# Kernel optimization log

Hardware: AMD Instinct MI355X
Metric: run time of the kernel (lower is better)

Reference implementation:

```python
import jax, jax.numpy as jnp
import numpy as np

N_NODES = 50000
N_EDGES = 800000
IN_FEATS = 128
OUT_FEATS = 16
NUM_HEADS = 8
NEG_SLOPE = 0.2


def setup_inputs() -> dict:
    key = jax.random.key(0)
    k1, k2, k3, k4, k5 = jax.random.split(key, 5)
    feat = jax.random.normal(k1, (N_NODES, IN_FEATS), dtype=jnp.float32)
    src = jax.random.randint(k2, (N_EDGES,), 0, N_NODES, dtype=jnp.int32)
    dst = jax.random.randint(k3, (N_EDGES,), 0, N_NODES, dtype=jnp.int32)
    # fc weight stored as [in, H*Dout] so y = x @ W (equivalent to torch Linear)
    W = jax.random.normal(k4, (IN_FEATS, NUM_HEADS * OUT_FEATS), dtype=jnp.float32) * 0.05
    attn_weights = jax.random.normal(k5, (2 * NUM_HEADS * OUT_FEATS,), dtype=jnp.float32) * 0.1
    bias = jnp.zeros((NUM_HEADS * OUT_FEATS,), dtype=jnp.float32)
    return {"feat": feat, "W": W, "attn_weights": attn_weights, "bias": bias,
            "src": src, "dst": dst}


def reference(feat, W, attn_weights, bias, src, dst):
    H, D = NUM_HEADS, OUT_FEATS
    N = feat.shape[0]
    # Linear projection: [N, H, D]
    h = (feat @ W).reshape(N, H, D)
    a = attn_weights.reshape(2, H, D)
    # per-node attention logits per head
    e_src = jnp.einsum("nhd,hd->nh", h, a[0])  # source side
    e_dst = jnp.einsum("nhd,hd->nh", h, a[1])  # destination side
    # per-edge scores: [E, H]
    e = e_src[src] + e_dst[dst]
    e = jnp.where(e > 0, e, NEG_SLOPE * e)  # LeakyReLU
    # segment softmax over incoming edges of each dst node
    m = jax.ops.segment_max(e, dst, num_segments=N)          # [N, H]
    m = jnp.where(jnp.isfinite(m), m, 0.0)
    ex = jnp.exp(e - m[dst])                                  # [E, H]
    denom = jax.ops.segment_sum(ex, dst, num_segments=N)     # [N, H]
    alpha = ex / jnp.where(denom[dst] > 0, denom[dst], 1.0)  # [E, H]
    # weighted aggregation of source features: [N, H, D]
    out = jax.ops.segment_sum(alpha[:, :, None] * h[src], dst, num_segments=N)
    out = out + bias.reshape(1, H, D)
    return out
```

## Files before the change

### kernel.cpp

```cpp
#include <hip/hip_runtime.h>
#include <hip/hip_bf16.h>

#define H_HEADS 8
#define D_OUT 16
#define C_FEATS 128
#define NEG_SLOPE 0.2f

typedef __attribute__((ext_vector_type(8))) short short8;
typedef __attribute__((ext_vector_type(4))) float f32x4;

__device__ inline unsigned short f2bf(float f) {
    __hip_bfloat16 b = __float2bfloat16(f);
    return *reinterpret_cast<unsigned short*>(&b);
}
__device__ inline float bf2f(unsigned short u) {
    return __uint_as_float((unsigned)u << 16);
}
__device__ inline float bf_lo(unsigned u) { return __uint_as_float(u << 16); }
__device__ inline float bf_hi(unsigned u) { return __uint_as_float(u & 0xffff0000u); }

__global__ __launch_bounds__(256) void k_prep(const float* __restrict__ W,
                                              unsigned short* __restrict__ Wfh,
                                              unsigned short* __restrict__ Wfl,
                                              int* __restrict__ deg, int N) {
    const int b = blockIdx.x, t = threadIdx.x;
    if (b < 8) {
        const int idx = b * 256 + t;
        const int frag = idx >> 6, lane = idx & 63;
        const int kc = frag >> 3, nt = frag & 7;
        const int kb = kc * 32 + ((lane >> 4) << 3);
        const int col = nt * 16 + (lane & 15);
        unsigned short hs[8], ls[8];
#pragma unroll
        for (int i = 0; i < 8; ++i) {
            const float x = W[(size_t)(kb + i) * C_FEATS + col];
            const unsigned short hh = f2bf(x);
            hs[i] = hh;
            ls[i] = f2bf(x - bf2f(hh));
        }
        uint4 uh, ul;
        uh.x = hs[0] | ((unsigned)hs[1] << 16);
        uh.y = hs[2] | ((unsigned)hs[3] << 16);
        uh.z = hs[4] | ((unsigned)hs[5] << 16);
        uh.w = hs[6] | ((unsigned)hs[7] << 16);
        ul.x = ls[0] | ((unsigned)ls[1] << 16);
        ul.y = ls[2] | ((unsigned)ls[3] << 16);
        ul.z = ls[4] | ((unsigned)ls[5] << 16);
        ul.w = ls[6] | ((unsigned)ls[7] << 16);
        *reinterpret_cast<uint4*>(&Wfh[(size_t)idx * 8]) = uh;
        *reinterpret_cast<uint4*>(&Wfl[(size_t)idx * 8]) = ul;
    } else {
        const int i = (b - 8) * 256 + t;
        if (i < N) deg[i] = 0;
    }
}

__global__ __launch_bounds__(256) void k_deg_rank(const int* __restrict__ dst,
                                                  int* __restrict__ deg,
                                                  int* __restrict__ rank, int E) {
    const int e = blockIdx.x * 256 + threadIdx.x;
    if (e < E)
        rank[e] = atomicAdd(&deg[dst[e]], 1);
}

__global__ __launch_bounds__(512) void k_gemm(
    const float* __restrict__ feat, const unsigned short* __restrict__ Wfh,
    const unsigned short* __restrict__ Wfl, const float* __restrict__ aw,
    unsigned short* __restrict__ h16, float* __restrict__ es,
    float* __restrict__ ed, int N) {
    const int t = threadIdx.x;
    __shared__ uint4 sW[4096];
    {
        const uint4* gh = reinterpret_cast<const uint4*>(Wfh);
        const uint4* gl = reinterpret_cast<const uint4*>(Wfl);
#pragma unroll
        for (int i = 0; i < 4; ++i) {
            const int j = t + i * 512;
            sW[j] = gh[j];
            sW[j + 2048] = gl[j];
        }
    }
    __syncthreads();

    const int bid = blockIdx.x;
    const int w = t >> 6, lane = t & 63;
    const int rbase = bid * 128 + w * 16;
    const int rowA = rbase + (lane & 15);
    const int ko = (lane >> 4) << 3;
    const bool rv = rowA < N;
    const float* fr = feat + (size_t)rowA * C_FEATS;

    f32x4 acc[8];
#pragma unroll
    for (int nt = 0; nt < 8; ++nt)
#pragma unroll
        for (int j = 0; j < 4; ++j) acc[nt][j] = 0.f;

#pragma unroll
    for (int kc = 0; kc < 4; ++kc) {
        float4 x0 = make_float4(0.f, 0.f, 0.f, 0.f), x1 = x0;
        if (rv) {
            x0 = *reinterpret_cast<const float4*>(fr + kc * 32 + ko);
            x1 = *reinterpret_cast<const float4*>(fr + kc * 32 + ko + 4);
        }
        const float xs[8] = {x0.x, x0.y, x0.z, x0.w, x1.x, x1.y, x1.z, x1.w};
        short8 ah, al;
#pragma unroll
        for (int i = 0; i < 8; ++i) {
            const unsigned short hh = f2bf(xs[i]);
            ah[i] = (short)hh;
            al[i] = (short)f2bf(xs[i] - bf2f(hh));
        }
#pragma unroll
        for (int nt = 0; nt < 8; ++nt) {
            const int fi = (kc * 8 + nt) * 64 + lane;
            const short8 bh = *reinterpret_cast<const short8*>(&sW[fi]);
            const short8 bl = *reinterpret_cast<const short8*>(&sW[fi + 2048]);
            acc[nt] = __builtin_amdgcn_mfma_f32_16x16x32_bf16(ah, bh, acc[nt], 0, 0, 0);
            acc[nt] = __builtin_amdgcn_mfma_f32_16x16x32_bf16(al, bh, acc[nt], 0, 0, 0);
            acc[nt] = __builtin_amdgcn_mfma_f32_16x16x32_bf16(ah, bl, acc[nt], 0, 0, 0);
        }
    }
    const int r0 = rbase + ((lane >> 4) << 2);
    const int colc = lane & 15;
#pragma unroll
    for (int nt = 0; nt < 8; ++nt) {
#pragma unroll
        for (int r = 0; r < 4; ++r) {
            const int row = r0 + r;
            if (row < N)
                h16[(size_t)row * C_FEATS + nt * 16 + colc] = f2bf(acc[nt][r]);
        }
    }
#pragma unroll
    for (int nt = 0; nt < 8; ++nt) {
        const float wa = aw[nt * 16 + colc];
        const float wb = aw[C_FEATS + nt * 16 + colc];
#pragma unroll
        for (int r = 0; r < 4; ++r) {
            float pe = acc[nt][r] * wa;
            float pd = acc[nt][r] * wb;
#pragma unroll
            for (int msk = 1; msk <= 8; msk <<= 1) {
                pe += __shfl_xor(pe, msk, 64);
                pd += __shfl_xor(pd, msk, 64);
            }
            const int row = r0 + r;
            if (colc == 0 && row < N) {
                es[(size_t)row * H_HEADS + nt] = pe;
                ed[(size_t)row * H_HEADS + nt] = pd;
            }
        }
    }
}

__global__ void k_bsum(const int* __restrict__ deg, int* __restrict__ bsum, int N) {
    int i = blockIdx.x * 256 + threadIdx.x;
    int v = (i < N) ? deg[i] : 0;
#pragma unroll
    for (int m = 1; m < 64; m <<= 1) v += __shfl_xor(v, m, 64);
    __shared__ int ws[4];
    if ((threadIdx.x & 63) == 0) ws[threadIdx.x >> 6] = v;
    __syncthreads();
    if (threadIdx.x == 0) bsum[blockIdx.x] = ws[0] + ws[1] + ws[2] + ws[3];
}

__device__ inline int block_scan_incl(int v) {
    int lane = threadIdx.x & 63, w = threadIdx.x >> 6;
    int x = v;
#pragma unroll
    for (int d = 1; d < 64; d <<= 1) {
        int u = __shfl_up(x, d, 64);
        if (lane >= d) x += u;
    }
    __shared__ int wsum[4];
    if (lane == 63) wsum[w] = x;
    __syncthreads();
    int add = 0;
    for (int k = 0; k < w; ++k) add += wsum[k];
    return x + add;
}

__global__ void k_scanb(const int* __restrict__ bsum, int* __restrict__ bpre,
                        int NB, int* __restrict__ offs, int N) {
    int t = threadIdx.x;
    int v = (t < NB) ? bsum[t] : 0;
    int incl = block_scan_incl(v);
    if (t < NB) bpre[t] = incl - v;
    if (t == NB - 1) offs[N] = incl;
}

__global__ void k_scanc(const int* __restrict__ deg, const int* __restrict__ bpre,
                        int* __restrict__ offs, int N) {
    int i = blockIdx.x * 256 + threadIdx.x;
    int v = (i < N) ? deg[i] : 0;
    int incl = block_scan_incl(v);
    int excl = incl - v + bpre[blockIdx.x];
    if (i < N) offs[i] = excl;
}

__global__ void k_scatter(const int* __restrict__ src, const int* __restrict__ dst,
                          const int* __restrict__ rank, const int* __restrict__ offs,
                          int* __restrict__ ssorted, int E) {
    int e = blockIdx.x * 256 + threadIdx.x;
    if (e < E)
        ssorted[offs[dst[e]] + rank[e]] = src[e];
}

__global__ __launch_bounds__(256) void k_agg(const unsigned short* __restrict__ h16,
                                             const float* __restrict__ es,
                                             const float* __restrict__ ed,
                                             const int* __restrict__ offs,
                                             const int* __restrict__ ssorted,
                                             const float* __restrict__ bias,
                                             float* __restrict__ out, int N) {
    const int wid = threadIdx.x >> 6, lane = threadIdx.x & 63;
    const int n = blockIdx.x * 4 + wid;
    if (n >= N) return;
    const int beg = offs[n];
    const int deg = offs[n + 1] - beg;

    const int hh = lane >> 3, j0 = lane & 7;
    const float edv = ed[(size_t)n * H_HEADS + hh];

    const int cl = lane & 15, q = lane >> 4;
    const int ah = cl >> 1;
    const int ab = ah << 3;
    float acc[8];
#pragma unroll
    for (int k = 0; k < 8; ++k) acc[k] = 0.f;

    float m = -1e30f, s = 0.f;

    if (deg <= 32) {
        int snc[4];
        float evc[4];
#pragma unroll
        for (int c = 0; c < 4; ++c) {
            const int j = c * 8 + j0;
            const bool va = (j < deg);
            int sn = 0;
            float ev = -1e30f;
            if (va) {
                sn = ssorted[beg + j];
                float t = es[(size_t)sn * H_HEADS + hh] + edv;
                ev = t > 0.f ? t : NEG_SLOPE * t;
                if (ev > m) {
                    s = s * __expf(m - ev) + 1.f;
                    m = ev;
                } else {
                    s += __expf(ev - m);
                }
            }
            snc[c] = sn;
            evc[c] = ev;
        }
#pragma unroll
        for (int msk = 1; msk < 8; msk <<= 1) {
            float mo = __shfl_xor(m, msk, 64);
            float so = __shfl_xor(s, msk, 64);
            float mn = fmaxf(m, mo);
            s = s * __expf(m - mn) + so * __expf(mo - mn);
            m = mn;
        }
        const float inv = (s > 0.f) ? 1.f / s : 0.f;

#pragma unroll
        for (int c = 0; c < 4; ++c) {
            const int cb = c * 8;
            if (cb >= deg) break;
            const float alpha = (cb + j0 < deg) ? __expf(evc[c] - m) * inv : 0.f;
            const int sn = snc[c];
            int rem = deg - cb; if (rem > 8) rem = 8;
#pragma unroll
            for (int e4 = 0; e4 < 2; ++e4) {
                if (4 * e4 >= rem) break;
                const int s0 = __shfl(sn, 4 * e4 + 0, 64);
                const int s1 = __shfl(sn, 4 * e4 + 1, 64);
                const int s2 = __shfl(sn, 4 * e4 + 2, 64);
                const int s3 = __shfl(sn, 4 * e4 + 3, 64);
                const int snq = (q == 0) ? s0 : (q == 1) ? s1 : (q == 2) ? s2 : s3;
                const float al = __shfl(alpha, ab + 4 * e4 + q, 64);
                const uint4 hv = *reinterpret_cast<const uint4*>(
                    &h16[(size_t)snq * C_FEATS + cl * 8]);
                acc[0] = fmaf(al, bf_lo(hv.x), acc[0]);
                acc[1] = fmaf(al, bf_hi(hv.x), acc[1]);
                acc[2] = fmaf(al, bf_lo(hv.y), acc[2]);
                acc[3] = fmaf(al, bf_hi(hv.y), acc[3]);
                acc[4] = fmaf(al, bf_lo(hv.z), acc[4]);
                acc[5] = fmaf(al, bf_hi(hv.z), acc[5]);
                acc[6] = fmaf(al, bf_lo(hv.w), acc[6]);
                acc[7] = fmaf(al, bf_hi(hv.w), acc[7]);
            }
        }
    } else {
        for (int e = j0; e < deg; e += 8) {
            int sn = ssorted[beg + e];
            float ev = es[(size_t)sn * H_HEADS + hh] + edv;
            ev = ev > 0.f ? ev : NEG_SLOPE * ev;
            if (ev > m) {
                s = s * __expf(m - ev) + 1.f;
                m = ev;
            } else {
                s += __expf(ev - m);
            }
        }
#pragma unroll
        for (int msk = 1; msk < 8; msk <<= 1) {
            float mo = __shfl_xor(m, msk, 64);
            float so = __shfl_xor(s, msk, 64);
            float mn = fmaxf(m, mo);
            s = s * __expf(m - mn) + so * __expf(mo - mn);
            m = mn;
        }
        const float inv = (s > 0.f) ? 1.f / s : 0.f;

        for (int cb = 0; cb < deg; cb += 8) {
            const int j = cb + j0;
            int sn = 0;
            float alpha = 0.f;
            if (j < deg) {
                sn = ssorted[beg + j];
                float t = es[(size_t)sn * H_HEADS + hh] + edv;
                t = t > 0.f ? t : NEG_SLOPE * t;
                alpha = __expf(t - m) * inv;
            }
            int rem = deg - cb; if (rem > 8) rem = 8;
#pragma unroll
            for (int e4 = 0; e4 < 2; ++e4) {
                if (4 * e4 >= rem) break;
                const int s0 = __shfl(sn, 4 * e4 + 0, 64);
                const int s1 = __shfl(sn, 4 * e4 + 1, 64);
                const int s2 = __shfl(sn, 4 * e4 + 2, 64);
                const int s3 = __shfl(sn, 4 * e4 + 3, 64);
                const int snq = (q == 0) ? s0 : (q == 1) ? s1 : (q == 2) ? s2 : s3;
                const float al = __shfl(alpha, ab + 4 * e4 + q, 64);
                const uint4 hv = *reinterpret_cast<const uint4*>(
                    &h16[(size_t)snq * C_FEATS + cl * 8]);
                acc[0] = fmaf(al, bf_lo(hv.x), acc[0]);
                acc[1] = fmaf(al, bf_hi(hv.x), acc[1]);
                acc[2] = fmaf(al, bf_lo(hv.y), acc[2]);
                acc[3] = fmaf(al, bf_hi(hv.y), acc[3]);
                acc[4] = fmaf(al, bf_lo(hv.z), acc[4]);
                acc[5] = fmaf(al, bf_hi(hv.z), acc[5]);
                acc[6] = fmaf(al, bf_lo(hv.w), acc[6]);
                acc[7] = fmaf(al, bf_hi(hv.w), acc[7]);
            }
        }
    }

#pragma unroll
    for (int k = 0; k < 8; ++k) {
        acc[k] += __shfl_xor(acc[k], 16, 64);
        acc[k] += __shfl_xor(acc[k], 32, 64);
    }
    if (q == 0) {
        const float4 b0 = *reinterpret_cast<const float4*>(&bias[cl * 8]);
        const float4 b1 = *reinterpret_cast<const float4*>(&bias[cl * 8 + 4]);
        float4 o0 = make_float4(acc[0] + b0.x, acc[1] + b0.y, acc[2] + b0.z, acc[3] + b0.w);
        float4 o1 = make_float4(acc[4] + b1.x, acc[5] + b1.y, acc[6] + b1.z, acc[7] + b1.w);
        *reinterpret_cast<float4*>(&out[(size_t)n * C_FEATS + cl * 8]) = o0;
        *reinterpret_cast<float4*>(&out[(size_t)n * C_FEATS + cl * 8 + 4]) = o1;
    }
}

extern "C" void kernel_launch(void* const* d_in, const int* in_sizes, int n_in,
                              void* d_out, int out_size, void* d_ws, size_t ws_size,
                              hipStream_t stream) {
    const float* feat = (const float*)d_in[0];
    const float* W    = (const float*)d_in[1];
    const float* aw   = (const float*)d_in[2];
    const float* bias = (const float*)d_in[3];
    const int*   src  = (const int*)d_in[4];
    const int*   dst  = (const int*)d_in[5];
    float* out = (float*)d_out;

    const int N = in_sizes[0] / C_FEATS;
    const int E = in_sizes[4];
    const int NB = (N + 255) / 256;
    const int GB = (N + 127) / 128;
    const int EB = (E + 255) / 256;

    char* p = (char*)d_ws;
    auto take = [&](size_t bytes) {
        char* q = p;
        p += (bytes + 255) & ~size_t(255);
        return q;
    };
    unsigned short* h16 = (unsigned short*)take((size_t)N * C_FEATS * 2);
    float* es      = (float*)take((size_t)N * H_HEADS * 4);
    float* edt     = (float*)take((size_t)N * H_HEADS * 4);
    int*   deg     = (int*)take((size_t)N * 4);
    int*   offs    = (int*)take((size_t)(N + 1) * 4);
    int*   bsum    = (int*)take((size_t)NB * 4);
    int*   bpre    = (int*)take((size_t)NB * 4);
    int*   ssorted = (int*)take((size_t)E * 4);
    int*   rank    = (int*)take((size_t)E * 4);
    unsigned short* Wfh = (unsigned short*)take((size_t)C_FEATS * C_FEATS * 2);
    unsigned short* Wfl = (unsigned short*)take((size_t)C_FEATS * C_FEATS * 2);
    (void)ws_size;

    k_prep<<<8 + NB, 256, 0, stream>>>(W, Wfh, Wfl, deg, N);
    k_deg_rank<<<EB, 256, 0, stream>>>(dst, deg, rank, E);
    k_gemm<<<GB, 512, 0, stream>>>(feat, Wfh, Wfl, aw, h16, es, edt, N);
    k_bsum<<<NB, 256, 0, stream>>>(deg, bsum, N);
    k_scanb<<<1, 256, 0, stream>>>(bsum, bpre, NB, offs, N);
    k_scanc<<<NB, 256, 0, stream>>>(deg, bpre, offs, N);
    k_scatter<<<EB, 256, 0, stream>>>(src, dst, rank, offs, ssorted, E);
    k_agg<<<(N + 3) / 4, 256, 0, stream>>>(h16, es, edt, offs, ssorted, bias, out, N);
}
```

Baseline: 133.6 us.

## Merge prep/degree and gemm/scatter launches, restructure small-degree aggregation

Folds the degree/rank atomic pass into the weight-prep kernel and replaces the degree zeroing with a memset. The GEMM kernel gains extra blocks that perform the CSR scatter, reordered after the scans so the two run in one launch. The small-degree aggregation path now uses a two-pass max/sum softmax and batches all feature gathers into registers before the FMAs, aiming to raise memory-level parallelism. The cost is more register pressure in k_agg, and scatter blocks now share a launch with GEMM blocks that reserve large shared memory.

```diff
diff --git a/kernel.cpp b/kernel.cpp
--- a/kernel.cpp
+++ b/kernel.cpp
@@ -19,10 +19,12 @@
 __device__ inline float bf_lo(unsigned u) { return __uint_as_float(u << 16); }
 __device__ inline float bf_hi(unsigned u) { return __uint_as_float(u & 0xffff0000u); }
 
-__global__ __launch_bounds__(256) void k_prep(const float* __restrict__ W,
-                                              unsigned short* __restrict__ Wfh,
-                                              unsigned short* __restrict__ Wfl,
-                                              int* __restrict__ deg, int N) {
+__global__ __launch_bounds__(256) void k_prep_deg(const float* __restrict__ W,
+                                                  unsigned short* __restrict__ Wfh,
+                                                  unsigned short* __restrict__ Wfl,
+                                                  const int* __restrict__ dst,
+                                                  int* __restrict__ deg,
+                                                  int* __restrict__ rank, int E) {
     const int b = blockIdx.x, t = threadIdx.x;
     if (b < 8) {
         const int idx = b * 256 + t;
@@ -50,25 +52,72 @@
         *reinterpret_cast<uint4*>(&Wfh[(size_t)idx * 8]) = uh;
         *reinterpret_cast<uint4*>(&Wfl[(size_t)idx * 8]) = ul;
     } else {
-        const int i = (b - 8) * 256 + t;
-        if (i < N) deg[i] = 0;
-    }
-}
-
-__global__ __launch_bounds__(256) void k_deg_rank(const int* __restrict__ dst,
-                                                  int* __restrict__ deg,
-                                                  int* __restrict__ rank, int E) {
-    const int e = blockIdx.x * 256 + threadIdx.x;
-    if (e < E)
-        rank[e] = atomicAdd(&deg[dst[e]], 1);
-}
-
-__global__ __launch_bounds__(512) void k_gemm(
+        const int e = (b - 8) * 256 + t;
+        if (e < E)
+            rank[e] = atomicAdd(&deg[dst[e]], 1);
+    }
+}
+
+__global__ void k_bsum(const int* __restrict__ deg, int* __restrict__ bsum, int N) {
+    int i = blockIdx.x * 256 + threadIdx.x;
+    int v = (i < N) ? deg[i] : 0;
+#pragma unroll
+    for (int m = 1; m < 64; m <<= 1) v += __shfl_xor(v, m, 64);
+    __shared__ int ws[4];
+    if ((threadIdx.x & 63) == 0) ws[threadIdx.x >> 6] = v;
+    __syncthreads();
+    if (threadIdx.x == 0) bsum[blockIdx.x] = ws[0] + ws[1] + ws[2] + ws[3];
+}
+
+__device__ inline int block_scan_incl(int v) {
+    int lane = threadIdx.x & 63, w = threadIdx.x >> 6;
+    int x = v;
+#pragma unroll
+    for (int d = 1; d < 64; d <<= 1) {
+        int u = __shfl_up(x, d, 64);
+        if (lane >= d) x += u;
+    }
+    __shared__ int wsum[4];
+    if (lane == 63) wsum[w] = x;
+    __syncthreads();
+    int add = 0;
+    for (int k = 0; k < w; ++k) add += wsum[k];
+    return x + add;
+}
+
+__global__ void k_scanb(const int* __restrict__ bsum, int* __restrict__ bpre,
+                        int NB, int* __restrict__ offs, int N) {
+    int t = threadIdx.x;
+    int v = (t < NB) ? bsum[t] : 0;
+    int incl = block_scan_incl(v);
+    if (t < NB) bpre[t] = incl - v;
+    if (t == NB - 1) offs[N] = incl;
+}
+
+__global__ void k_scanc(const int* __restrict__ deg, const int* __restrict__ bpre,
+                        int* __restrict__ offs, int N) {
+    int i = blockIdx.x * 256 + threadIdx.x;
+    int v = (i < N) ? deg[i] : 0;
+    int incl = block_scan_incl(v);
+    int excl = incl - v + bpre[blockIdx.x];
+    if (i < N) offs[i] = excl;
+}
+
+__global__ __launch_bounds__(512) void k_gemm_scatter(
     const float* __restrict__ feat, const unsigned short* __restrict__ Wfh,
     const unsigned short* __restrict__ Wfl, const float* __restrict__ aw,
     unsigned short* __restrict__ h16, float* __restrict__ es,
-    float* __restrict__ ed, int N) {
+    float* __restrict__ ed, const int* __restrict__ src,
+    const int* __restrict__ dst, const int* __restrict__ rank,
+    const int* __restrict__ offs, int* __restrict__ ssorted,
+    int N, int E, int GB) {
     const int t = threadIdx.x;
+    if ((int)blockIdx.x >= GB) {
+        const int e = (blockIdx.x - GB) * 512 + t;
+        if (e < E)
+            ssorted[offs[dst[e]] + rank[e]] = src[e];
+        return;
+    }
     __shared__ uint4 sW[4096];
     {
         const uint4* gh = reinterpret_cast<const uint4*>(Wfh);
@@ -152,59 +201,6 @@
             }
         }
     }
-}
-
-__global__ void k_bsum(const int* __restrict__ deg, int* __restrict__ bsum, int N) {
-    int i = blockIdx.x * 256 + threadIdx.x;
-    int v = (i < N) ? deg[i] : 0;
-#pragma unroll
-    for (int m = 1; m < 64; m <<= 1) v += __shfl_xor(v, m, 64);
-    __shared__ int ws[4];
-    if ((threadIdx.x & 63) == 0) ws[threadIdx.x >> 6] = v;
-    __syncthreads();
-    if (threadIdx.x == 0) bsum[blockIdx.x] = ws[0] + ws[1] + ws[2] + ws[3];
-}
-
-__device__ inline int block_scan_incl(int v) {
-    int lane = threadIdx.x & 63, w = threadIdx.x >> 6;
-    int x = v;
-#pragma unroll
-    for (int d = 1; d < 64; d <<= 1) {
-        int u = __shfl_up(x, d, 64);
-        if (lane >= d) x += u;
-    }
-    __shared__ int wsum[4];
-    if (lane == 63) wsum[w] = x;
-    __syncthreads();
-    int add = 0;
-    for (int k = 0; k < w; ++k) add += wsum[k];
-    return x + add;
-}
-
-__global__ void k_scanb(const int* __restrict__ bsum, int* __restrict__ bpre,
-                        int NB, int* __restrict__ offs, int N) {
-    int t = threadIdx.x;
-    int v = (t < NB) ? bsum[t] : 0;
-    int incl = block_scan_incl(v);
-    if (t < NB) bpre[t] = incl - v;
-    if (t == NB - 1) offs[N] = incl;
-}
-
-__global__ void k_scanc(const int* __restrict__ deg, const int* __restrict__ bpre,
-                        int* __restrict__ offs, int N) {
-    int i = blockIdx.x * 256 + threadIdx.x;
-    int v = (i < N) ? deg[i] : 0;
-    int incl = block_scan_incl(v);
-    int excl = incl - v + bpre[blockIdx.x];
-    if (i < N) offs[i] = excl;
-}
-
-__global__ void k_scatter(const int* __restrict__ src, const int* __restrict__ dst,
-                          const int* __restrict__ rank, const int* __restrict__ offs,
-                          int* __restrict__ ssorted, int E) {
-    int e = blockIdx.x * 256 + threadIdx.x;
-    if (e < E)
-        ssorted[offs[dst[e]] + rank[e]] = src[e];
 }
 
 __global__ __launch_bounds__(256) void k_agg(const unsigned short* __restrict__ h16,
@@ -230,30 +226,88 @@
 #pragma unroll
     for (int k = 0; k < 8; ++k) acc[k] = 0.f;
 
-    float m = -1e30f, s = 0.f;
-
     if (deg <= 32) {
         int snc[4];
-        float evc[4];
 #pragma unroll
         for (int c = 0; c < 4; ++c) {
             const int j = c * 8 + j0;
-            const bool va = (j < deg);
-            int sn = 0;
-            float ev = -1e30f;
-            if (va) {
-                sn = ssorted[beg + j];
-                float t = es[(size_t)sn * H_HEADS + hh] + edv;
-                ev = t > 0.f ? t : NEG_SLOPE * t;
-                if (ev > m) {
-                    s = s * __expf(m - ev) + 1.f;
-                    m = ev;
-                } else {
-                    s += __expf(ev - m);
+            snc[c] = (j < deg) ? ssorted[beg + j] : 0;
+        }
+        float evc[4];
+#pragma unroll
+        for (int c = 0; c < 4; ++c) {
+            const int j = c * 8 + j0;
+            if (j < deg) {
+                float tv = es[(size_t)snc[c] * H_HEADS + hh] + edv;
+                evc[c] = tv > 0.f ? tv : NEG_SLOPE * tv;
+            } else {
+                evc[c] = -1e30f;
+            }
+        }
+        float m = fmaxf(fmaxf(evc[0], evc[1]), fmaxf(evc[2], evc[3]));
+#pragma unroll
+        for (int msk = 1; msk < 8; msk <<= 1)
+            m = fmaxf(m, __shfl_xor(m, msk, 64));
+        const float t0 = __expf(evc[0] - m), t1 = __expf(evc[1] - m);
+        const float t2 = __expf(evc[2] - m), t3 = __expf(evc[3] - m);
+        float s = t0 + t1 + t2 + t3;
+#pragma unroll
+        for (int msk = 1; msk < 8; msk <<= 1)
+            s += __shfl_xor(s, msk, 64);
+        const float inv = (s > 0.f) ? 1.f / s : 0.f;
+        const float alc[4] = {t0 * inv, t1 * inv, t2 * inv, t3 * inv};
+
+        uint4 hv[8];
+        float alv[8];
+#pragma unroll
+        for (int c = 0; c < 4; ++c) {
+#pragma unroll
+            for (int e4 = 0; e4 < 2; ++e4) {
+                const int idx = c * 2 + e4;
+                const int base = c * 8 + e4 * 4;
+                if (base < deg) {
+                    const int s0 = __shfl(snc[c], 4 * e4 + 0, 64);
+                    const int s1 = __shfl(snc[c], 4 * e4 + 1, 64);
+                    const int s2 = __shfl(snc[c], 4 * e4 + 2, 64);
+                    const int s3 = __shfl(snc[c], 4 * e4 + 3, 64);
+                    const int snq = (q == 0) ? s0 : (q == 1) ? s1 : (q == 2) ? s2 : s3;
+                    alv[idx] = __shfl(alc[c], ab + 4 * e4 + q, 64);
+                    hv[idx] = *reinterpret_cast<const uint4*>(
+                        &h16[(size_t)snq * C_FEATS + cl * 8]);
                 }
             }
-            snc[c] = sn;
-            evc[c] = ev;
+        }
+#pragma unroll
+        for (int c = 0; c < 4; ++c) {
+#pragma unroll
+            for (int e4 = 0; e4 < 2; ++e4) {
+                const int idx = c * 2 + e4;
+                const int base = c * 8 + e4 * 4;
+                if (base < deg) {
+                    const float al = alv[idx];
+                    acc[0] = fmaf(al, bf_lo(hv[idx].x), acc[0]);
+                    acc[1] = fmaf(al, bf_hi(hv[idx].x), acc[1]);
+                    acc[2] = fmaf(al, bf_lo(hv[idx].y), acc[2]);
+                    acc[3] = fmaf(al, bf_hi(hv[idx].y), acc[3]);
+                    acc[4] = fmaf(al, bf_lo(hv[idx].z), acc[4]);
+                    acc[5] = fmaf(al, bf_hi(hv[idx].z), acc[5]);
+                    acc[6] = fmaf(al, bf_lo(hv[idx].w), acc[6]);
+                    acc[7] = fmaf(al, bf_hi(hv[idx].w), acc[7]);
+                }
+            }
+        }
+    } else {
+        float m = -1e30f, s = 0.f;
+        for (int e = j0; e < deg; e += 8) {
+            int sn = ssorted[beg + e];
+            float ev = es[(size_t)sn * H_HEADS + hh] + edv;
+            ev = ev > 0.f ? ev : NEG_SLOPE * ev;
+            if (ev > m) {
+                s = s * __expf(m - ev) + 1.f;
+                m = ev;
+            } else {
+                s += __expf(ev - m);
+            }
         }
 #pragma unroll
         for (int msk = 1; msk < 8; msk <<= 1) {
@@ -265,12 +319,16 @@
         }
         const float inv = (s > 0.f) ? 1.f / s : 0.f;
 
-#pragma unroll
-        for (int c = 0; c < 4; ++c) {
-            const int cb = c * 8;
-            if (cb >= deg) break;
-            const float alpha = (cb + j0 < deg) ? __expf(evc[c] - m) * inv : 0.f;
-            const int sn = snc[c];
+        for (int cb = 0; cb < deg; cb += 8) {
+            const int j = cb + j0;
+            int sn = 0;
+            float alpha = 0.f;
+            if (j < deg) {
+                sn = ssorted[beg + j];
+                float tv = es[(size_t)sn * H_HEADS + hh] + edv;
+                tv = tv > 0.f ? tv : NEG_SLOPE * tv;
+                alpha = __expf(tv - m) * inv;
+            }
             int rem = deg - cb; if (rem > 8) rem = 8;
 #pragma unroll
             for (int e4 = 0; e4 < 2; ++e4) {
@@ -293,60 +351,6 @@
                 acc[7] = fmaf(al, bf_hi(hv.w), acc[7]);
             }
         }
-    } else {
-        for (int e = j0; e < deg; e += 8) {
-            int sn = ssorted[beg + e];
-            float ev = es[(size_t)sn * H_HEADS + hh] + edv;
-            ev = ev > 0.f ? ev : NEG_SLOPE * ev;
-            if (ev > m) {
-                s = s * __expf(m - ev) + 1.f;
-                m = ev;
-            } else {
-                s += __expf(ev - m);
-            }
-        }
-#pragma unroll
-        for (int msk = 1; msk < 8; msk <<= 1) {
-            float mo = __shfl_xor(m, msk, 64);
-            float so = __shfl_xor(s, msk, 64);
-            float mn = fmaxf(m, mo);
-            s = s * __expf(m - mn) + so * __expf(mo - mn);
-            m = mn;
-        }
-        const float inv = (s > 0.f) ? 1.f / s : 0.f;
-
-        for (int cb = 0; cb < deg; cb += 8) {
-            const int j = cb + j0;
-            int sn = 0;
-            float alpha = 0.f;
-            if (j < deg) {
-                sn = ssorted[beg + j];
-                float t = es[(size_t)sn * H_HEADS + hh] + edv;
-                t = t > 0.f ? t : NEG_SLOPE * t;
-                alpha = __expf(t - m) * inv;
-            }
-            int rem = deg - cb; if (rem > 8) rem = 8;
-#pragma unroll
-            for (int e4 = 0; e4 < 2; ++e4) {
-                if (4 * e4 >= rem) break;
-                const int s0 = __shfl(sn, 4 * e4 + 0, 64);
-                const int s1 = __shfl(sn, 4 * e4 + 1, 64);
-                const int s2 = __shfl(sn, 4 * e4 + 2, 64);
-                const int s3 = __shfl(sn, 4 * e4 + 3, 64);
-                const int snq = (q == 0) ? s0 : (q == 1) ? s1 : (q == 2) ? s2 : s3;
-                const float al = __shfl(alpha, ab + 4 * e4 + q, 64);
-                const uint4 hv = *reinterpret_cast<const uint4*>(
-                    &h16[(size_t)snq * C_FEATS + cl * 8]);
-                acc[0] = fmaf(al, bf_lo(hv.x), acc[0]);
-                acc[1] = fmaf(al, bf_hi(hv.x), acc[1]);
-                acc[2] = fmaf(al, bf_lo(hv.y), acc[2]);
-                acc[3] = fmaf(al, bf_hi(hv.y), acc[3]);
-                acc[4] = fmaf(al, bf_lo(hv.z), acc[4]);
-                acc[5] = fmaf(al, bf_hi(hv.z), acc[5]);
-                acc[6] = fmaf(al, bf_lo(hv.w), acc[6]);
-                acc[7] = fmaf(al, bf_hi(hv.w), acc[7]);
-            }
-        }
     }
 
 #pragma unroll
@@ -380,6 +384,7 @@
     const int NB = (N + 255) / 256;
     const int GB = (N + 127) / 128;
     const int EB = (E + 255) / 256;
+    const int EB2 = (E + 511) / 512;
 
     char* p = (char*)d_ws;
     auto take = [&](size_t bytes) {
@@ -400,12 +405,13 @@
     unsigned short* Wfl = (unsigned short*)take((size_t)C_FEATS * C_FEATS * 2);
     (void)ws_size;
 
-    k_prep<<<8 + NB, 256, 0, stream>>>(W, Wfh, Wfl, deg, N);
-    k_deg_rank<<<EB, 256, 0, stream>>>(dst, deg, rank, E);
-    k_gemm<<<GB, 512, 0, stream>>>(feat, Wfh, Wfl, aw, h16, es, edt, N);
+    hipMemsetAsync(deg, 0, (size_t)N * 4, stream);
+    k_prep_deg<<<8 + EB, 256, 0, stream>>>(W, Wfh, Wfl, dst, deg, rank, E);
     k_bsum<<<NB, 256, 0, stream>>>(deg, bsum, N);
     k_scanb<<<1, 256, 0, stream>>>(bsum, bpre, NB, offs, N);
     k_scanc<<<NB, 256, 0, stream>>>(deg, bpre, offs, N);
-    k_scatter<<<EB, 256, 0, stream>>>(src, dst, rank, offs, ssorted, E);
+    k_gemm_scatter<<<GB + EB2, 512, 0, stream>>>(feat, Wfh, Wfl, aw, h16, es, edt,
+                                                 src, dst, rank, offs, ssorted,
+                                                 N, E, GB);
     k_agg<<<(N + 3) / 4, 256, 0, stream>>>(h16, es, edt, offs, ssorted, bias, out, N);
 }
```

Result: faster. 119.9 us (-10.3%).
